# Performance work log

Hardware: AMD Instinct MI355X
Metric: run time of the kernel (lower is better)

## Reference

```python
import jax, jax.numpy as jnp
import numpy as np

LRELU = 0.01  # torch nn.LeakyReLU default slope

def _lrelu(x):
    return jnp.where(x >= 0, x, LRELU * x)

def setup_inputs() -> dict:
    key = jax.random.key(0)
    ks = jax.random.split(key, 10)
    B, Cin, Cout, H, W, K, FD, LAT = 16, 256, 256, 64, 64, 3, 128, 128
    y = jax.random.normal(ks[0], (B, Cin, H, W), jnp.float32)
    finger = jax.random.randint(ks[1], (B, FD), 0, 2).astype(jnp.float32)
    ori_weight = jax.random.normal(ks[2], (Cout, Cin, K, K), jnp.float32) * 0.05
    w_mask = jax.random.normal(ks[3], (Cout, Cin, 1, 1), jnp.float32)
    f_weight = ori_weight[None]  # param initialized as 1*ori_weight, shape [1,Cout,Cin,K,K]
    style_w1 = jax.random.normal(ks[4], (LAT, FD), jnp.float32) / np.sqrt(FD)
    style_w2 = jax.random.normal(ks[5], (2 * Cin * K * K, LAT), jnp.float32) / np.sqrt(LAT)
    ori_bias = jax.random.normal(ks[6], (Cout,), jnp.float32) * 0.05
    b_mask = jax.random.normal(ks[7], (Cout,), jnp.float32)
    f_bias = ori_bias[None]  # [1,Cout]
    bias_w1 = jax.random.normal(ks[8], (Cout, FD), jnp.float32) / np.sqrt(FD)
    bias_w2 = jax.random.normal(ks[9], (Cout, Cout), jnp.float32) / np.sqrt(Cout)
    return dict(y=y, finger=finger, ori_weight=ori_weight, w_mask=w_mask,
                f_weight=f_weight, style_w1=style_w1, style_w2=style_w2,
                ori_bias=ori_bias, b_mask=b_mask, f_bias=f_bias,
                bias_w1=bias_w1, bias_w2=bias_w2)

def reference(y, finger, ori_weight, w_mask, f_weight, style_w1, style_w2,
              ori_bias, b_mask, f_bias, bias_w1, bias_w2):
    B = y.shape[0]
    Cout, Cin, K, _ = ori_weight.shape
    relu6 = lambda v: jnp.clip(v, 0.0, 6.0)
    # mask blending coefficients (w_mask broadcasts over the KxK taps, as in .repeat)
    f_w_weight = (6.0 - relu6(w_mask)) / 6.0          # [Cout,Cin,1,1]
    f_w_bias = (6.0 - relu6(b_mask)) / 6.0            # [Cout]
    mean_ori = ori_weight.mean()
    std_ori = jnp.std(ori_weight, ddof=1)             # torch .std() is unbiased
    # ApplyStyle: finger -> LAT -> 2*Cin*K*K scale/shift applied to f_weight
    h = _lrelu(finger @ style_w1.T)                   # [B,LAT]
    style = (h @ style_w2.T).reshape(B, 2, 1, Cin, K, K)
    s_weight = f_weight * (style[:, 0] + 1.0) + style[:, 1]  # [B,Cout,Cin,K,K]
    fw = f_w_weight[None]
    w1 = (1.0 - fw) * ori_weight[None] + fw * s_weight
    # per-sample whole-tensor re-standardization to ori stats
    mean = w1.mean(axis=(1, 2, 3, 4), keepdims=True)
    std = jnp.std(w1, axis=(1, 2, 3, 4), keepdims=True, ddof=1)
    w2 = (w1 - mean) / std * std_ori + mean_ori
    new_weight = (1.0 - fw) * ori_weight[None] + fw * w2      # [B,Cout,Cin,K,K]
    # per-sample bias
    s_bias = f_bias * _lrelu(_lrelu(finger @ bias_w1.T) @ bias_w2.T)  # [B,Cout]
    new_bias = (1.0 - f_w_bias) * ori_bias + f_w_bias * s_bias        # [B,Cout]
    pad = K // 2
    def conv_one(xi, wi, bi):
        o = jax.lax.conv_general_dilated(xi[None], wi, (1, 1),
                                         [(pad, pad), (pad, pad)],
                                         dimension_numbers=('NCHW', 'OIHW', 'NCHW'))
        return o[0] + bi[:, None, None]
    return jax.vmap(conv_one)(y, new_weight, new_bias)   # [B,Cout,H,W]
```

## Files before the change

kernel.cpp:

```cpp
#include <hip/hip_runtime.h>
#include <math.h>

#define LSLOPE 0.01f

__device__ __forceinline__ float lrelu(float x){ return x >= 0.f ? x : LSLOPE * x; }

typedef __attribute__((ext_vector_type(8))) short short8;
typedef __attribute__((ext_vector_type(4))) float f32x4;

__device__ __forceinline__ unsigned short f2bf(float f){
  union { float f; unsigned u; } v; v.f = f;
  unsigned r = v.u + 0x7FFFu + ((v.u >> 16) & 1u);
  return (unsigned short)(r >> 16);
}

__device__ __forceinline__ void gload_lds16(const unsigned short* g, unsigned short* l){
  __builtin_amdgcn_global_load_lds((const __attribute__((address_space(1))) unsigned int*)(g),
                                   (__attribute__((address_space(3))) unsigned int*)(l), 16, 0, 0);
}

constexpr int B    = 16;
constexpr int CIN  = 256;
constexpr int COUT = 256;
constexpr int HH   = 64;
constexpr int WW   = 64;
constexpr int FD   = 128;
constexpr int LAT  = 128;
constexpr int WPS  = CIN * 9;
constexpr int WTOT = COUT * WPS;
constexpr int HP   = 66;

constexpr int OFF_C     = 64;
constexpr int OFF_STYLE = OFF_C + 11 * WPS;
constexpr int OFF_NBIAS = OFF_STYLE + B * 2 * WPS;
constexpr int OFF_NW    = OFF_NBIAS + B * COUT;
constexpr int OFF_YTR   = OFF_NW + (B * 9 * COUT * CIN) / 2;

constexpr int PADT = 264;
constexpr int NB_CF = 9;
constexpr int NB_SB = B * 18 + B;
constexpr int NB_YT = HP * B;

__global__ __launch_bounds__(256) void k_prep1(const float* __restrict__ y, unsigned short* __restrict__ ytrp,
                                               const float* __restrict__ ow, const float* __restrict__ fwgt,
                                               const float* __restrict__ wmask, float* __restrict__ C,
                                               const float* __restrict__ finger, const float* __restrict__ sw1,
                                               const float* __restrict__ sw2, float* __restrict__ style,
                                               const float* __restrict__ bw1, const float* __restrict__ bw2,
                                               const float* __restrict__ fbias, const float* __restrict__ bmask,
                                               const float* __restrict__ obias, float* __restrict__ nbias){
  __shared__ __align__(16) char shraw[64 * PADT * 2];
  const int blk = blockIdx.x;
  const int tid = threadIdx.x;

  if (blk < NB_CF){
    const int rem = blk * 256 + tid;
    const int ic = rem / 9;
    float a_ow = 0.f, q_ow = 0.f, ab = 0.f, qb = 0.f;
    float a1 = 0.f, a2 = 0.f, d1 = 0.f, d2 = 0.f, d3 = 0.f, d4 = 0.f, d5 = 0.f;
    for (int oc = 0; oc < COUT; ++oc){
      float w = ow[(size_t)oc * WPS + rem];
      float f = fwgt[(size_t)oc * WPS + rem];
      float m = wmask[oc * CIN + ic];
      float fw = (6.f - fminf(fmaxf(m, 0.f), 6.f)) * (1.f / 6.f);
      float base = w + fw * (f - w);
      float c1 = fw * f, c2 = fw;
      a_ow += w; q_ow += w * w;
      ab += base; qb += base * base;
      a1 += c1; a2 += c2;
      d1 += c1 * c1; d2 += c2 * c2; d3 += base * c1; d4 += base * c2; d5 += c1 * c2;
    }
    C[(size_t)0  * WPS + rem] = a_ow; C[(size_t)1  * WPS + rem] = q_ow;
    C[(size_t)2  * WPS + rem] = ab;   C[(size_t)3  * WPS + rem] = qb;
    C[(size_t)4  * WPS + rem] = a1;   C[(size_t)5  * WPS + rem] = a2;
    C[(size_t)6  * WPS + rem] = d1;   C[(size_t)7  * WPS + rem] = d2;
    C[(size_t)8  * WPS + rem] = d3;   C[(size_t)9  * WPS + rem] = d4;
    C[(size_t)10 * WPS + rem] = d5;
  } else if (blk < NB_CF + NB_SB){
    float* sh = (float*)shraw;
    const int blk2 = blk - NB_CF;
    if (blk2 < B * 18){
      const int b = blk2 / 18, j0 = (blk2 - b * 18) * 256;
      if (tid < LAT){
        float a = 0.f;
        const float* fg = finger + b * FD;
        const float* w = sw1 + (size_t)tid * FD;
        for (int f = 0; f < FD; ++f) a += fg[f] * w[f];
        sh[tid] = lrelu(a);
      }
      __syncthreads();
      const int j = j0 + tid;
      float a = 0.f;
      const float* w2 = sw2 + (size_t)j * LAT;
      for (int l = 0; l < LAT; ++l) a += sh[l] * w2[l];
      style[(size_t)b * 2 * WPS + j] = a;
    } else {
      const int b = blk2 - B * 18, o = tid;
      float acc = 0.f;
      for (int f = 0; f < FD; ++f) acc += finger[b * FD + f] * bw1[o * FD + f];
      sh[o] = lrelu(acc);
      __syncthreads();
      float t = 0.f;
      for (int c = 0; c < COUT; ++c) t += sh[c] * bw2[o * COUT + c];
      t = lrelu(t);
      float sb = fbias[o] * t;
      float fwb = (6.f - fminf(fmaxf(bmask[o], 0.f), 6.f)) * (1.f / 6.f);
      nbias[b * COUT + o] = (1.f - fwb) * obias[o] + fwb * sb;
    }
  } else {
    unsigned short* t = (unsigned short*)shraw;
    const int blk3 = blk - NB_CF - NB_SB;
    const int ghp = blk3 % HP, b = blk3 / HP;
    unsigned short* dst = ytrp + ((size_t)b * HP + ghp) * HP * CIN;
    if (ghp == 0 || ghp == HP - 1){
      for (int c = tid; c < HP * CIN / 8; c += 256) ((uint4*)dst)[c] = (uint4){0, 0, 0, 0};
      return;
    }
    const int h = ghp - 1;
    const float* src = y + (size_t)b * CIN * HH * WW + h * WW;
    #pragma unroll
    for (int k = 0; k < 16; ++k){
      int idx = tid + k * 256;
      int ic = idx >> 4, w4 = (idx & 15) * 4;
      float4 v = *(const float4*)(src + (size_t)ic * HH * WW + w4);
      t[(w4 + 0) * PADT + ic] = f2bf(v.x);
      t[(w4 + 1) * PADT + ic] = f2bf(v.y);
      t[(w4 + 2) * PADT + ic] = f2bf(v.z);
      t[(w4 + 3) * PADT + ic] = f2bf(v.w);
    }
    __syncthreads();
    for (int c = tid; c < HP * CIN / 8; c += 256){
      int gwp = c >> 5, icg = (c & 31) * 8;
      uint4 v = (uint4){0, 0, 0, 0};
      if (gwp >= 1 && gwp <= 64) v = *(const uint4*)(&t[(gwp - 1) * PADT + icg]);
      ((uint4*)dst)[c] = v;
    }
  }
}

__global__ __launch_bounds__(256) void k_new_weight5(const float* __restrict__ ow, const float* __restrict__ fwgt,
                                                     const float* __restrict__ wmask, const float* __restrict__ style,
                                                     const float* __restrict__ C, unsigned short* __restrict__ nw){
  __shared__ float ows[WPS];
  __shared__ float fws[WPS];
  __shared__ float sts[2 * WPS];
  __shared__ float red[2][4];
  __shared__ float bcast[4];
  const int bi = blockIdx.x, oc = blockIdx.y;
  const int tid = threadIdx.x;
  const int lane = tid & 63, wid = tid >> 6;
  const float* owr = ow + (size_t)oc * WPS;
  const float* fwr = fwgt + (size_t)oc * WPS;
  for (int i = tid; i < WPS; i += 256){ ows[i] = owr[i]; fws[i] = fwr[i]; }
  const float fw = (6.f - fminf(fmaxf(wmask[oc * CIN + tid], 0.f), 6.f)) * (1.f / 6.f);

  {
    float so = 0.f, qo = 0.f;
    for (int k = 0; k < 9; ++k){
      int rem = k * 256 + tid;
      so += C[0 * WPS + rem]; qo += C[1 * WPS + rem];
    }
    for (int o = 32; o > 0; o >>= 1){ so += __shfl_down(so, o); qo += __shfl_down(qo, o); }
    if (lane == 0){ red[0][wid] = so; red[1][wid] = qo; }
    __syncthreads();
    if (tid == 0){
      const float N = (float)WTOT;
      float SO = red[0][0] + red[0][1] + red[0][2] + red[0][3];
      float QO = red[1][0] + red[1][1] + red[1][2] + red[1][3];
      bcast[2] = SO / N;
      bcast[3] = sqrtf((QO - SO * SO / N) / (N - 1.f));
    }
    __syncthreads();
  }
  const float mean_ori = bcast[2], std_ori = bcast[3];

  #pragma unroll 1
  for (int bb = 0; bb < 4; ++bb){
    const int b = bi * 4 + bb;
    __syncthreads();
    const float* st = style + (size_t)b * 2 * WPS;
    for (int i = tid; i < 2 * WPS; i += 256) sts[i] = st[i];
    __syncthreads();
    float s = 0.f, q = 0.f;
    for (int k = 0; k < 9; ++k){
      int rem = k * 256 + tid;
      float ab = C[2 * WPS + rem], qb = C[3 * WPS + rem];
      float a1 = C[4 * WPS + rem], a2 = C[5 * WPS + rem];
      float d1 = C[6 * WPS + rem], d2 = C[7 * WPS + rem];
      float d3 = C[8 * WPS + rem], d4 = C[9 * WPS + rem], d5 = C[10 * WPS + rem];
      float s0 = sts[rem], s1 = sts[WPS + rem];
      s += ab + s0 * a1 + s1 * a2;
      q += qb + s0 * s0 * d1 + s1 * s1 * d2 + 2.f * (s0 * d3 + s1 * d4 + s0 * s1 * d5);
    }
    for (int o = 32; o > 0; o >>= 1){ s += __shfl_down(s, o); q += __shfl_down(q, o); }
    if (lane == 0){ red[0][wid] = s; red[1][wid] = q; }
    __syncthreads();
    if (tid == 0){
      const float N = (float)WTOT;
      float S = red[0][0] + red[0][1] + red[0][2] + red[0][3];
      float Q = red[1][0] + red[1][1] + red[1][2] + red[1][3];
      bcast[0] = S / N;
      bcast[1] = sqrtf((Q - S * S / N) / (N - 1.f));
    }
    __syncthreads();
    const float bm = bcast[0], bs = bcast[1];
    #pragma unroll
    for (int t = 0; t < 9; ++t){
      int rem = tid * 9 + t;
      float owv = ows[rem];
      float sw = fws[rem] * (sts[rem] + 1.f) + sts[WPS + rem];
      float w1 = owv + fw * (sw - owv);
      float w2 = (w1 - bm) / bs * std_ori + mean_ori;
      nw[((size_t)(b * 9 + t) * COUT + oc) * CIN + tid] = f2bf(owv + fw * (w2 - owv));
    }
  }
}

__global__ __launch_bounds__(256, 2) void k_conv_mfma13(const unsigned short* __restrict__ ytrp,
                                                        const unsigned short* __restrict__ nw,
                                                        const float* __restrict__ nbias,
                                                        float* __restrict__ out){
  constexpr int WASTRIDE = 3 * 128 * 32;
  constexpr int YTSTRIDE = 144 * 32;
  __shared__ __align__(16) unsigned short Wa[2 * WASTRIDE];
  __shared__ __align__(16) unsigned short Yt[2 * YTSTRIDE];
  __shared__ float bsh[128];

  const int bid = blockIdx.x;
  const int xcd = bid & 7, idx = bid >> 3;
  const int b   = ((idx >> 6) << 3) | xcd;
  const int rem6 = idx & 63;
  const int oc0 = (rem6 & 1) * 128;
  const int hwt = rem6 >> 1;
  const int tid = threadIdx.x;
  const int lane = tid & 63, wid = tid >> 6;
  const int wr = wid >> 1, wc = wid & 1;
  const int hw0 = hwt * 128;
  const int h0  = hwt * 2;

  if (tid < 128) bsh[tid] = nbias[b * COUT + oc0 + tid];

  f32x4 acc[4][4];
  #pragma unroll
  for (int i = 0; i < 4; ++i)
    #pragma unroll
    for (int j = 0; j < 4; ++j) acc[i][j] = (f32x4){0.f, 0.f, 0.f, 0.f};

  const unsigned short* nwb = nw + ((size_t)(b * 9) * COUT + oc0) * CIN;
  const unsigned short* ytb = ytrp + (size_t)b * HP * HP * CIN;

  int a_tap[6], a_go[6], a_lo[6];
  #pragma unroll
  for (int s = 0; s < 6; ++s){
    int I = wid + 4 * s;
    int tap = I >> 3, rowbase = (I & 7) * 16;
    int row = rowbase + (lane >> 2), p = lane & 3;
    int g = p ^ ((row >> 1) & 3);
    a_tap[s] = tap;
    a_go[s]  = row * CIN + g * 8;
    a_lo[s]  = (tap * 128 + rowbase) * 32;
  }
  int y_go[3], y_lo[3]; bool y_has[3];
  #pragma unroll
  for (int s = 0; s < 3; ++s){
    int I = wid + 4 * s;
    y_has[s] = (I < 9);
    int Ic = y_has[s] ? I : 0;
    int site = Ic * 16 + (lane >> 2);
    int srow = (site >= 72) ? 1 : 0;
    int scol = site - srow * 72;
    int gwp  = scol > 65 ? 65 : scol;
    int p = lane & 3, g = p ^ ((site >> 1) & 3);
    y_go[s] = ((h0 + srow + 1) * HP + gwp) * CIN + g * 8;
    y_lo[s] = Ic * 16 * 32;
  }

  const int gq = lane >> 4;
  int a_rb[4];
  #pragma unroll
  for (int mi = 0; mi < 4; ++mi){
    int r = wr * 64 + mi * 16 + (lane & 15);
    a_rb[mi] = r * 64 + ((gq ^ ((r >> 1) & 3)) << 4);
  }
  int b_site[4];
  #pragma unroll
  for (int ni = 0; ni < 4; ++ni)
    b_site[ni] = wc * 72 + ni * 16 + (lane & 15);

  #define STAGE(BUF, IT)                                                            \
    {                                                                               \
      const int dhb = (IT) >> 3;                                                    \
      const int ic0s = ((IT) & 7) * 32;                                             \
      unsigned short* wb = &Wa[(BUF) * WASTRIDE];                                   \
      unsigned short* yb = &Yt[(BUF) * YTSTRIDE];                                   \
      const unsigned short* ybase = ytb + (ptrdiff_t)(dhb - 1) * HP * CIN + ic0s;   \
      _Pragma("unroll")                                                             \
      for (int s = 0; s < 3; ++s)                                                   \
        if (y_has[s]) gload_lds16(ybase + y_go[s], yb + y_lo[s]);                   \
      const unsigned short* atap = nwb + (size_t)(dhb * 3) * COUT * CIN + ic0s;     \
      _Pragma("unroll")                                                             \
      for (int s = 0; s < 6; ++s)                                                   \
        gload_lds16(atap + (size_t)a_tap[s] * COUT * CIN + a_go[s], wb + a_lo[s]);  \
    }

  #define COMPUTE(BUF)                                                              \
    {                                                                               \
      const char* wap = (const char*)&Wa[(BUF) * WASTRIDE];                         \
      const char* ytp = (const char*)&Yt[(BUF) * YTSTRIDE];                         \
      _Pragma("unroll")                                                             \
      for (int tap = 0; tap < 3; ++tap){                                            \
        short8 af[4];                                                               \
        _Pragma("unroll")                                                           \
        for (int mi = 0; mi < 4; ++mi)                                              \
          af[mi] = *(const short8*)(wap + tap * 8192 + a_rb[mi]);                   \
        _Pragma("unroll")                                                           \
        for (int ni = 0; ni < 4; ++ni){                                             \
          const int site = b_site[ni] + tap;                                        \
          const int boff = (site << 6) + ((gq ^ ((site >> 1) & 3)) << 4);           \
          const short8 bf = *(const short8*)(ytp + boff);                           \
          _Pragma("unroll")                                                         \
          for (int mi = 0; mi < 4; ++mi)                                            \
            acc[mi][ni] = __builtin_amdgcn_mfma_f32_16x16x32_bf16(af[mi], bf, acc[mi][ni], 0, 0, 0); \
        }                                                                           \
      }                                                                             \
    }

  STAGE(0, 0);
  STAGE(1, 1);
  #pragma unroll 1
  for (int it = 0; it < 24; ++it){
    if (it < 23) asm volatile("s_waitcnt vmcnt(8)" ::: "memory");
    else         asm volatile("s_waitcnt vmcnt(0)" ::: "memory");
    asm volatile("s_barrier" ::: "memory");
    COMPUTE(it & 1);
    asm volatile("s_barrier" ::: "memory");
    if (it + 2 < 24){ STAGE(it & 1, it + 2); }
  }
  #undef STAGE
  #undef COMPUTE

  const int col_l = lane & 15, row_l = (lane >> 4) * 4;
  #pragma unroll
  for (int mi = 0; mi < 4; ++mi){
    #pragma unroll
    for (int r = 0; r < 4; ++r){
      const int ocl = wr * 64 + mi * 16 + row_l + r;
      const float bb = bsh[ocl];
      float* op = out + ((size_t)(b * COUT + oc0 + ocl)) * (HH * WW) + hw0 + wc * 64;
      #pragma unroll
      for (int ni = 0; ni < 4; ++ni)
        op[ni * 16 + col_l] = acc[mi][ni][r] + bb;
    }
  }
}

extern "C" void kernel_launch(void* const* d_in, const int* in_sizes, int n_in,
                              void* d_out, int out_size, void* d_ws, size_t ws_size,
                              hipStream_t stream){
  const float* y      = (const float*)d_in[0];
  const float* finger = (const float*)d_in[1];
  const float* ow     = (const float*)d_in[2];
  const float* wmask  = (const float*)d_in[3];
  const float* fwgt   = (const float*)d_in[4];
  const float* sw1    = (const float*)d_in[5];
  const float* sw2    = (const float*)d_in[6];
  const float* obias  = (const float*)d_in[7];
  const float* bmask  = (const float*)d_in[8];
  const float* fbias  = (const float*)d_in[9];
  const float* bw1    = (const float*)d_in[10];
  const float* bw2    = (const float*)d_in[11];
  float* out = (float*)d_out;
  float* ws  = (float*)d_ws;

  float* C     = ws + OFF_C;
  float* style = ws + OFF_STYLE;
  float* nbias = ws + OFF_NBIAS;
  unsigned short* nw   = (unsigned short*)(ws + OFF_NW);
  unsigned short* ytrp = (unsigned short*)(ws + OFF_YTR);

  k_prep1<<<NB_CF + NB_SB + NB_YT, 256, 0, stream>>>(y, ytrp, ow, fwgt, wmask, C,
                                                     finger, sw1, sw2, style,
                                                     bw1, bw2, fbias, bmask, obias, nbias);
  k_new_weight5<<<dim3(4, COUT), 256, 0, stream>>>(ow, fwgt, wmask, style, C, nw);
  k_conv_mfma13<<<1024, 256, 0, stream>>>(ytrp, nw, nbias, out);
}
```

Before: 144.9 us.

## Enlarge conv tile to 256x256 with 512-thread blocks and MFMA priority

```diff
diff --git a/kernel.cpp b/kernel.cpp
--- a/kernel.cpp
+++ b/kernel.cpp
@@ -216,58 +216,56 @@
   }
 }
 
-__global__ __launch_bounds__(256, 2) void k_conv_mfma13(const unsigned short* __restrict__ ytrp,
+__global__ __launch_bounds__(512, 2) void k_conv_mfma14(const unsigned short* __restrict__ ytrp,
                                                         const unsigned short* __restrict__ nw,
                                                         const float* __restrict__ nbias,
                                                         float* __restrict__ out){
-  constexpr int WASTRIDE = 3 * 128 * 32;
-  constexpr int YTSTRIDE = 144 * 32;
+  constexpr int WASTRIDE = 3 * 256 * 32;
+  constexpr int YTSTRIDE = 4 * 72 * 32;
   __shared__ __align__(16) unsigned short Wa[2 * WASTRIDE];
   __shared__ __align__(16) unsigned short Yt[2 * YTSTRIDE];
-  __shared__ float bsh[128];
+  __shared__ float bsh[256];
 
   const int bid = blockIdx.x;
   const int xcd = bid & 7, idx = bid >> 3;
-  const int b   = ((idx >> 6) << 3) | xcd;
-  const int rem6 = idx & 63;
-  const int oc0 = (rem6 & 1) * 128;
-  const int hwt = rem6 >> 1;
+  const int b   = ((idx >> 4) << 3) | xcd;
+  const int hwt = idx & 15;
   const int tid = threadIdx.x;
   const int lane = tid & 63, wid = tid >> 6;
-  const int wr = wid >> 1, wc = wid & 1;
-  const int hw0 = hwt * 128;
-  const int h0  = hwt * 2;
-
-  if (tid < 128) bsh[tid] = nbias[b * COUT + oc0 + tid];
-
-  f32x4 acc[4][4];
-  #pragma unroll
-  for (int i = 0; i < 4; ++i)
+  const int wm = wid >> 2, wn = wid & 3;
+  const int hw0 = hwt * 256;
+  const int h0  = hwt * 4;
+
+  if (tid < 256) bsh[tid] = nbias[b * COUT + tid];
+
+  f32x4 acc[8][4];
+  #pragma unroll
+  for (int i = 0; i < 8; ++i)
     #pragma unroll
     for (int j = 0; j < 4; ++j) acc[i][j] = (f32x4){0.f, 0.f, 0.f, 0.f};
 
-  const unsigned short* nwb = nw + ((size_t)(b * 9) * COUT + oc0) * CIN;
+  const unsigned short* nwb = nw + (size_t)(b * 9) * COUT * CIN;
   const unsigned short* ytb = ytrp + (size_t)b * HP * HP * CIN;
 
   int a_tap[6], a_go[6], a_lo[6];
   #pragma unroll
   for (int s = 0; s < 6; ++s){
-    int I = wid + 4 * s;
-    int tap = I >> 3, rowbase = (I & 7) * 16;
+    int I = wid + 8 * s;
+    int tap = I >> 4, rowbase = (I & 15) * 16;
     int row = rowbase + (lane >> 2), p = lane & 3;
     int g = p ^ ((row >> 1) & 3);
     a_tap[s] = tap;
     a_go[s]  = row * CIN + g * 8;
-    a_lo[s]  = (tap * 128 + rowbase) * 32;
+    a_lo[s]  = (tap * 256 + rowbase) * 32;
   }
   int y_go[3], y_lo[3]; bool y_has[3];
   #pragma unroll
   for (int s = 0; s < 3; ++s){
-    int I = wid + 4 * s;
-    y_has[s] = (I < 9);
+    int I = wid + 8 * s;
+    y_has[s] = (I < 18);
     int Ic = y_has[s] ? I : 0;
     int site = Ic * 16 + (lane >> 2);
-    int srow = (site >= 72) ? 1 : 0;
+    int srow = site / 72;
     int scol = site - srow * 72;
     int gwp  = scol > 65 ? 65 : scol;
     int p = lane & 3, g = p ^ ((site >> 1) & 3);
@@ -276,16 +274,16 @@
   }
 
   const int gq = lane >> 4;
-  int a_rb[4];
-  #pragma unroll
-  for (int mi = 0; mi < 4; ++mi){
-    int r = wr * 64 + mi * 16 + (lane & 15);
+  int a_rb[8];
+  #pragma unroll
+  for (int mi = 0; mi < 8; ++mi){
+    int r = wm * 128 + mi * 16 + (lane & 15);
     a_rb[mi] = r * 64 + ((gq ^ ((r >> 1) & 3)) << 4);
   }
   int b_site[4];
   #pragma unroll
   for (int ni = 0; ni < 4; ++ni)
-    b_site[ni] = wc * 72 + ni * 16 + (lane & 15);
+    b_site[ni] = wn * 72 + ni * 16 + (lane & 15);
 
   #define STAGE(BUF, IT)                                                            \
     {                                                                               \
@@ -309,19 +307,23 @@
       const char* ytp = (const char*)&Yt[(BUF) * YTSTRIDE];                         \
       _Pragma("unroll")                                                             \
       for (int tap = 0; tap < 3; ++tap){                                            \
-        short8 af[4];                                                               \
+        short8 af[8];                                                               \
         _Pragma("unroll")                                                           \
-        for (int mi = 0; mi < 4; ++mi)                                              \
-          af[mi] = *(const short8*)(wap + tap * 8192 + a_rb[mi]);                   \
+        for (int mi = 0; mi < 8; ++mi)                                              \
+          af[mi] = *(const short8*)(wap + tap * 16384 + a_rb[mi]);                  \
+        short8 bfr[4];                                                              \
         _Pragma("unroll")                                                           \
         for (int ni = 0; ni < 4; ++ni){                                             \
           const int site = b_site[ni] + tap;                                        \
-          const int boff = (site << 6) + ((gq ^ ((site >> 1) & 3)) << 4);           \
-          const short8 bf = *(const short8*)(ytp + boff);                           \
+          bfr[ni] = *(const short8*)(ytp + (site << 6) + ((gq ^ ((site >> 1) & 3)) << 4)); \
+        }                                                                           \
+        __builtin_amdgcn_s_setprio(1);                                              \
+        _Pragma("unroll")                                                           \
+        for (int ni = 0; ni < 4; ++ni)                                              \
           _Pragma("unroll")                                                         \
-          for (int mi = 0; mi < 4; ++mi)                                            \
-            acc[mi][ni] = __builtin_amdgcn_mfma_f32_16x16x32_bf16(af[mi], bf, acc[mi][ni], 0, 0, 0); \
-        }                                                                           \
+          for (int mi = 0; mi < 8; ++mi)                                            \
+            acc[mi][ni] = __builtin_amdgcn_mfma_f32_16x16x32_bf16(af[mi], bfr[ni], acc[mi][ni], 0, 0, 0); \
+        __builtin_amdgcn_s_setprio(0);                                              \
       }                                                                             \
     }
 
@@ -341,12 +343,12 @@
 
   const int col_l = lane & 15, row_l = (lane >> 4) * 4;
   #pragma unroll
-  for (int mi = 0; mi < 4; ++mi){
+  for (int mi = 0; mi < 8; ++mi){
     #pragma unroll
     for (int r = 0; r < 4; ++r){
-      const int ocl = wr * 64 + mi * 16 + row_l + r;
+      const int ocl = wm * 128 + mi * 16 + row_l + r;
       const float bb = bsh[ocl];
-      float* op = out + ((size_t)(b * COUT + oc0 + ocl)) * (HH * WW) + hw0 + wc * 64;
+      float* op = out + ((size_t)(b * COUT + ocl)) * (HH * WW) + hw0 + wn * 64;
       #pragma unroll
       for (int ni = 0; ni < 4; ++ni)
         op[ni * 16 + col_l] = acc[mi][ni][r] + bb;
@@ -382,5 +384,5 @@
                                                      finger, sw1, sw2, style,
                                                      bw1, bw2, fbias, bmask, obias, nbias);
   k_new_weight5<<<dim3(4, COUT), 256, 0, stream>>>(ow, fwgt, wmask, style, C, nw);
-  k_conv_mfma13<<<1024, 256, 0, stream>>>(ytrp, nw, nbias, out);
-}
+  k_conv_mfma14<<<256, 512, 0, stream>>>(ytrp, nw, nbias, out);
+}
```

New measurement: 146.0 us. No clear change (+0.8%).
